# Performance work log

Hardware: AMD Instinct MI355X
Metric: run time of the kernel (lower is better)

## Reference

```python
import jax, jax.numpy as jnp
import numpy as np
from jax import lax

B, L, K, OUT = 16384, 8192, 2, 128
L3 = L - 3 * (K - 1)  # 8189, length after 3 valid convs


def setup_inputs() -> dict:
    key = jax.random.key(0)
    ks = jax.random.split(key, 9)
    return {
        "x": jax.random.normal(ks[0], (B, 1, L), jnp.float32),
        "w1": jax.random.normal(ks[1], (1, 1, K), jnp.float32),
        "b1": jax.random.normal(ks[2], (1,), jnp.float32),
        "w2": jax.random.normal(ks[3], (1, 1, K), jnp.float32),
        "b2": jax.random.normal(ks[4], (1,), jnp.float32),
        "w3": jax.random.normal(ks[5], (1, 1, K), jnp.float32),
        "b3": jax.random.normal(ks[6], (1,), jnp.float32),
        "W": jax.random.normal(ks[7], (OUT, L3), jnp.float32) * 0.02,
        "b": jax.random.normal(ks[8], (OUT,), jnp.float32),
    }


def _conv1d(x, w, b):
    # x: [B, 1, L_in], w: [1, 1, K] (OIW), valid padding, stride 1
    y = lax.conv_general_dilated(x, w, window_strides=(1,), padding="VALID",
                                 dimension_numbers=("NCW", "OIW", "NCW"))
    return y + b[None, :, None]


def reference(x, w1, b1, w2, b2, w3, b3, W, b):
    h = jax.nn.relu(_conv1d(x, w1, b1))
    h = jax.nn.relu(_conv1d(h, w2, b2))
    h = jax.nn.relu(_conv1d(h, w3, b3))
    flat = h.reshape(h.shape[0], -1)          # [B, L3]
    return flat @ W.T + b                     # [B, OUT]
```

## Files before the change

### kernel.cpp

```cpp
#include <hip/hip_runtime.h>
#include <hip/hip_bf16.h>

typedef __attribute__((ext_vector_type(8))) short short8;
typedef __attribute__((ext_vector_type(8))) unsigned short ushort8;
typedef __attribute__((ext_vector_type(4))) float f32x4;

#define LIN  8192
#define L3V  8189
#define NOUT 128
#define KP   8192
#define BM   64
#define BK   128
#define NT   (KP / BK)
#define PITCH (BK + 8)

static __device__ __forceinline__ unsigned short f2bf(float f) {
    union { float f; unsigned u; } c; c.f = f;
    unsigned r = c.u + 0x7FFFu + ((c.u >> 16) & 1u);
    return (unsigned short)(r >> 16);
}

__global__ void wprep(const float* __restrict__ W, unsigned short* __restrict__ Wb) {
    int idx = blockIdx.x * 256 + threadIdx.x;
    int n = idx >> 13;
    int k = idx & (KP - 1);
    float v = (k < L3V) ? W[(size_t)n * L3V + k] : 0.0f;
    Wb[idx] = f2bf(v);
}

__global__ __launch_bounds__(512, 2) void fused(
    const float* __restrict__ x,
    const float* __restrict__ w1, const float* __restrict__ b1,
    const float* __restrict__ w2, const float* __restrict__ b2,
    const float* __restrict__ w3, const float* __restrict__ b3,
    const unsigned short* __restrict__ Wb,
    const float* __restrict__ bias,
    float* __restrict__ out)
{
    __shared__ unsigned short hA[2][BM * PITCH];
    __shared__ unsigned short wA[2][NOUT * PITCH];

    const int tid  = threadIdx.x;
    const int row0 = blockIdx.x * BM;

    const float w10 = w1[0], w11 = w1[1], cb1 = b1[0];
    const float w20 = w2[0], w21 = w2[1], cb2 = b2[0];
    const float w30 = w3[0], w31 = w3[1], cb3 = b3[0];

    const int srow = tid >> 3;
    const int scol = (tid & 7) * 16;
    const float* xrow = x + (size_t)(row0 + srow) * LIN;

    const int wn = tid >> 2;
    const int wq = tid & 3;

    const int lane = tid & 63;
    const int wid  = tid >> 6;
    const int wr   = wid >> 1;
    const int wc   = wid & 1;
    const int l15  = lane & 15;
    const int koff = (lane >> 4) * 8;
    const int arow_off = (wr * 16 + l15) * PITCH + koff;

    f32x4 acc[4];
    #pragma unroll
    for (int f = 0; f < 4; ++f) acc[f] = (f32x4){0.f, 0.f, 0.f, 0.f};

    auto stage = [&](int t, int s) {
        const int k0 = t * BK;
        const int gk = k0 + scol;
        float xv[20];
        if (gk + 20 <= LIN) {
            #pragma unroll
            for (int q = 0; q < 5; ++q) {
                const float4 v = *reinterpret_cast<const float4*>(xrow + gk + q * 4);
                xv[q*4+0] = v.x; xv[q*4+1] = v.y; xv[q*4+2] = v.z; xv[q*4+3] = v.w;
            }
        } else {
            #pragma unroll
            for (int j = 0; j < 20; ++j)
                xv[j] = (gk + j < LIN) ? xrow[gk + j] : 0.0f;
        }
        float h1[18];
        #pragma unroll
        for (int j = 0; j < 18; ++j)
            h1[j] = fmaxf(fmaf(w10, xv[j], fmaf(w11, xv[j+1], cb1)), 0.0f);
        float h2[17];
        #pragma unroll
        for (int j = 0; j < 17; ++j)
            h2[j] = fmaxf(fmaf(w20, h1[j], fmaf(w21, h1[j+1], cb2)), 0.0f);
        ushort8 hp[2];
        #pragma unroll
        for (int j = 0; j < 16; ++j) {
            float h3 = fmaxf(fmaf(w30, h2[j], fmaf(w31, h2[j+1], cb3)), 0.0f);
            unsigned short u = (gk + j < L3V) ? f2bf(h3) : (unsigned short)0;
            hp[j >> 3][j & 7] = u;
        }
        ushort8* hd = reinterpret_cast<ushort8*>(&hA[s][srow * PITCH + scol]);
        hd[0] = hp[0];
        hd[1] = hp[1];
        const ushort8* wsrc = reinterpret_cast<const ushort8*>(Wb + (size_t)wn * KP + k0 + wq * 32);
        ushort8* wdst = reinterpret_cast<ushort8*>(&wA[s][wn * PITCH + wq * 32]);
        #pragma unroll
        for (int i = 0; i < 4; ++i) wdst[i] = wsrc[i];
    };

    stage(0, 0);
    int sel = 0;
    for (int t = 0; t < NT; ++t) {
        __syncthreads();
        if (t + 1 < NT) stage(t + 1, sel ^ 1);
        const unsigned short* hB = hA[sel];
        const unsigned short* wB = wA[sel];
        #pragma unroll
        for (int kk = 0; kk < BK; kk += 32) {
            const short8 af = *reinterpret_cast<const short8*>(&hB[arow_off + kk]);
            #pragma unroll
            for (int f = 0; f < 4; ++f) {
                const int bn = wc * 64 + f * 16 + l15;
                const short8 bf = *reinterpret_cast<const short8*>(&wB[bn * PITCH + kk + koff]);
                acc[f] = __builtin_amdgcn_mfma_f32_16x16x32_bf16(af, bf, acc[f], 0, 0, 0);
            }
        }
        sel ^= 1;
    }

    #pragma unroll
    for (int f = 0; f < 4; ++f) {
        const int col = wc * 64 + f * 16 + l15;
        const float bv = bias[col];
        #pragma unroll
        for (int j = 0; j < 4; ++j) {
            const int grow = row0 + wr * 16 + (lane >> 4) * 4 + j;
            out[(size_t)grow * NOUT + col] = acc[f][j] + bv;
        }
    }
}

extern "C" void kernel_launch(void* const* d_in, const int* in_sizes, int n_in,
                              void* d_out, int out_size, void* d_ws, size_t ws_size,
                              hipStream_t stream) {
    const float* x  = (const float*)d_in[0];
    const float* w1 = (const float*)d_in[1];
    const float* b1 = (const float*)d_in[2];
    const float* w2 = (const float*)d_in[3];
    const float* b2 = (const float*)d_in[4];
    const float* w3 = (const float*)d_in[5];
    const float* b3 = (const float*)d_in[6];
    const float* W  = (const float*)d_in[7];
    const float* b  = (const float*)d_in[8];
    float* out = (float*)d_out;
    unsigned short* Wb = (unsigned short*)d_ws;

    wprep<<<dim3((NOUT * KP) / 256), dim3(256), 0, stream>>>(W, Wb);
    fused<<<dim3(16384 / BM), dim3(512), 0, stream>>>(
        x, w1, b1, w2, b2, w3, b3, Wb, b, out);
}
```

Baseline: 169.3 us.

## Split staging into register prefetch and LDS store to overlap global loads

The staging step is split into a global-to-register load and a compute-and-store into LDS. Loads for tile t+2 are issued after the MFMA loop of tile t and held in registers across the next iteration, so global latency overlaps compute. The sync moves to the end of each iteration. The tail path now uses vector loads with zero padding instead of per-element guarded loads. The cost is more live registers under launch_bounds(512,2), which could cause spills or lower occupancy.

New measurement: 142.9 us. 15.6% less time.

```diff
diff --git a/kernel.cpp b/kernel.cpp
--- a/kernel.cpp
+++ b/kernel.cpp
@@ -53,6 +53,7 @@
 
     const int wn = tid >> 2;
     const int wq = tid & 3;
+    const unsigned short* wrow = Wb + (size_t)wn * KP + wq * 32;
 
     const int lane = tid & 63;
     const int wid  = tid >> 6;
@@ -66,10 +67,11 @@
     #pragma unroll
     for (int f = 0; f < 4; ++f) acc[f] = (f32x4){0.f, 0.f, 0.f, 0.f};
 
-    auto stage = [&](int t, int s) {
-        const int k0 = t * BK;
-        const int gk = k0 + scol;
-        float xv[20];
+    float   xv[20];
+    ushort8 wv[4];
+
+    auto stage_load = [&](int t) {
+        const int gk = t * BK + scol;
         if (gk + 20 <= LIN) {
             #pragma unroll
             for (int q = 0; q < 5; ++q) {
@@ -78,9 +80,19 @@
             }
         } else {
             #pragma unroll
-            for (int j = 0; j < 20; ++j)
-                xv[j] = (gk + j < LIN) ? xrow[gk + j] : 0.0f;
+            for (int q = 0; q < 4; ++q) {
+                const float4 v = *reinterpret_cast<const float4*>(xrow + gk + q * 4);
+                xv[q*4+0] = v.x; xv[q*4+1] = v.y; xv[q*4+2] = v.z; xv[q*4+3] = v.w;
+            }
+            xv[16] = 0.f; xv[17] = 0.f; xv[18] = 0.f; xv[19] = 0.f;
         }
+        const ushort8* wsrc = reinterpret_cast<const ushort8*>(wrow + t * BK);
+        #pragma unroll
+        for (int i = 0; i < 4; ++i) wv[i] = wsrc[i];
+    };
+
+    auto stage_store = [&](int t, int s) {
+        const int gk = t * BK + scol;
         float h1[18];
         #pragma unroll
         for (int j = 0; j < 18; ++j)
@@ -99,17 +111,18 @@
         ushort8* hd = reinterpret_cast<ushort8*>(&hA[s][srow * PITCH + scol]);
         hd[0] = hp[0];
         hd[1] = hp[1];
-        const ushort8* wsrc = reinterpret_cast<const ushort8*>(Wb + (size_t)wn * KP + k0 + wq * 32);
         ushort8* wdst = reinterpret_cast<ushort8*>(&wA[s][wn * PITCH + wq * 32]);
         #pragma unroll
-        for (int i = 0; i < 4; ++i) wdst[i] = wsrc[i];
+        for (int i = 0; i < 4; ++i) wdst[i] = wv[i];
     };
 
-    stage(0, 0);
+    stage_load(0);
+    stage_store(0, 0);
+    stage_load(1);
+    __syncthreads();
+
     int sel = 0;
     for (int t = 0; t < NT; ++t) {
-        __syncthreads();
-        if (t + 1 < NT) stage(t + 1, sel ^ 1);
         const unsigned short* hB = hA[sel];
         const unsigned short* wB = wA[sel];
         #pragma unroll
@@ -122,6 +135,9 @@
                 acc[f] = __builtin_amdgcn_mfma_f32_16x16x32_bf16(af, bf, acc[f], 0, 0, 0);
             }
         }
+        if (t + 1 < NT) stage_store(t + 1, sel ^ 1);
+        if (t + 2 < NT) stage_load(t + 2);
+        __syncthreads();
         sel ^= 1;
     }
 
```
